# Optimization experiments

Hardware: AMD Instinct MI355X
Metric: run time of the kernel (lower is better)

Reference implementation:

```python
import jax, jax.numpy as jnp
import numpy as np
import math

S, D, H, HD = 2048, 1280, 16, 80  # seq_len, embed_dim, num_heads, head_dim


def setup_inputs() -> dict:
    key = jax.random.key(0)
    k1, k2, k3, k4, k5, k6 = jax.random.split(key, 6)
    hidden_states = jax.random.normal(k1, (S, D), dtype=jnp.float32)
    # 4 equal-length segments (e.g. 4 images of 512 patches)
    cu_seqlens = jnp.array([0, 512, 1024, 1536, 2048], dtype=jnp.int32)
    # RoPE theta*position angles, [S, HD//2]
    rotary_pos_emb = jax.random.uniform(k2, (S, HD // 2), dtype=jnp.float32) * 10.0
    qkv_w = jax.random.normal(k3, (3 * D, D), dtype=jnp.float32) * 0.02
    qkv_b = jax.random.normal(k4, (3 * D,), dtype=jnp.float32) * 0.02
    proj_w = jax.random.normal(k5, (D, D), dtype=jnp.float32) * 0.02
    proj_b = jax.random.normal(k6, (D,), dtype=jnp.float32) * 0.02
    return {"hidden_states": hidden_states, "cu_seqlens": cu_seqlens,
            "rotary_pos_emb": rotary_pos_emb, "qkv_w": qkv_w, "qkv_b": qkv_b,
            "proj_w": proj_w, "proj_b": proj_b}


def _rotate_half(x):
    x1, x2 = jnp.split(x, 2, axis=-1)
    return jnp.concatenate([-x2, x1], axis=-1)


def _square_mask(n, seq, dtype):
    # faithful translation of rewrite_loop_for_square_mask on a full-min mask
    neg = jnp.finfo(dtype).min
    mask = jnp.full((1, n, n), neg, dtype=dtype)
    r = jnp.arange(n)
    less0 = (r[:, None] < seq[None, :]).astype(jnp.int32)
    less = less0.sum(axis=-1, keepdims=True) + 1            # [n,1] segment label
    sq = less * less.T                                       # [n,n]
    c1 = jnp.logical_or(seq.min() == 0, less != less.max())
    c2 = jnp.logical_or(seq.max() == n, less != less.min())
    look = (c1 & c2).astype(jnp.int32) * less
    filt = (sq != look ** 2).astype(dtype)                   # 0 inside blocks, 1 outside
    return mask * filt


def reference(hidden_states, cu_seqlens, rotary_pos_emb, qkv_w, qkv_b, proj_w, proj_b):
    seq_len = hidden_states.shape[0]
    qkv = hidden_states @ qkv_w.T + qkv_b                    # [S, 3D]
    qkv = qkv.reshape(seq_len, 3, H, HD)
    q, k, v = qkv[:, 0], qkv[:, 1], qkv[:, 2]                # [S, H, HD]

    # rotary_pos_emb path: emb = cat(rope, rope), cos/sin broadcast over heads
    emb = jnp.concatenate([rotary_pos_emb, rotary_pos_emb], axis=-1)  # [S, HD]
    cos = jnp.cos(emb)[:, None, :]                           # [S, 1, HD]
    sin = jnp.sin(emb)[:, None, :]
    q = q * cos + _rotate_half(q) * sin
    k = k * cos + _rotate_half(k) * sin

    mask = _square_mask(seq_len, cu_seqlens, q.dtype)        # [1, S, S]

    qh = q.transpose(1, 0, 2)                                # [H, S, HD]
    kh = k.transpose(1, 0, 2)
    vh = v.transpose(1, 0, 2)

    attn = jnp.einsum('hqd,hkd->hqk', qh, kh) / math.sqrt(HD)  # [H, S, S]
    attn = attn + mask
    attn = jax.nn.softmax(attn.astype(jnp.float32), axis=-1).astype(q.dtype)
    out = jnp.einsum('hqk,hkd->hqd', attn, vh)               # [H, S, HD]
    out = out.transpose(1, 0, 2).reshape(seq_len, -1)        # [S, D]
    return out @ proj_w.T + proj_b
```

## Files before the change

### kernel.cpp

```cpp
#include <hip/hip_runtime.h>


typedef unsigned short u16;
typedef short short8 __attribute__((ext_vector_type(8)));
typedef float floatx4 __attribute__((ext_vector_type(4)));
typedef u16 ushort4v __attribute__((ext_vector_type(4)));
typedef float float4v __attribute__((ext_vector_type(4)));
typedef float float2v __attribute__((ext_vector_type(2)));

#define S_LEN 2048
#define DMODEL 1280
#define NHEAD 16
#define HDIM 80
#define HDIM_P 96
#define SEGS 4
#define SEG_LEN 512
#define QSCALE 0.11180339887498948f

__device__ __forceinline__ float b2f(u16 u) {
  union { unsigned int i; float f; } v; v.i = ((unsigned int)u) << 16; return v.f;
}
__device__ __forceinline__ u16 f2b(float f) {
  union { float f; unsigned int i; } v; v.f = f;
  unsigned int i = v.i;
  return (u16)((i + 0x7FFFu + ((i >> 16) & 1u)) >> 16);
}

__device__ __forceinline__ void load_lds16(const u16* g, u16* l) {
  __builtin_amdgcn_global_load_lds(
      (const __attribute__((address_space(1))) unsigned int*)g,
      (__attribute__((address_space(3))) unsigned int*)l, 16, 0, 0);
}

__device__ __forceinline__ unsigned int rope_perm(unsigned int j) {
  if (j >= 2560u) return j;
  unsigned int sec = j / 1280u;
  unsigned int jj = j - sec * 1280u;
  unsigned int h = jj / 80u, d = jj - h * 80u;
  unsigned int dp = (d < 40u) ? (2u * d) : (2u * (d - 40u) + 1u);
  return sec * 1280u + h * 80u + dp;
}

__global__ __launch_bounds__(256) void convert_all(
    const void* __restrict__ s_hid, const void* __restrict__ s_qw,
    const void* __restrict__ s_pw,  const void* __restrict__ s_rope,
    const void* __restrict__ s_qb,  const void* __restrict__ s_pb,
    u16* __restrict__ d_hid, u16* __restrict__ d_qw, u16* __restrict__ d_pw,
    u16* __restrict__ d_qb, u16* __restrict__ d_pb,
    int* __restrict__ flag_out, float* __restrict__ cs_tab,
    float* __restrict__ sn_tab) {
  unsigned int w = ((const unsigned int*)s_rope)[threadIdx.x & 63];
  int is_f32 = __any((int)((w >> 15) & 1));
  if (blockIdx.x == 0 && threadIdx.x == 0) *flag_out = is_f32;

  unsigned int qi = blockIdx.x * 256 + threadIdx.x;

  if (qi >= 2295040u) {
    unsigned int ti = qi - 2295040u;
    float ang = is_f32 ? ((const float*)s_rope)[ti]
                       : b2f(((const u16*)s_rope)[ti]);
    cs_tab[ti] = cosf(ang);
    sn_tab[ti] = sinf(ang);
    return;
  }

  if (qi >= 2293760u && qi < 2294720u) {
    unsigned int off = qi - 2293760u;
    ushort4v o;
    if (is_f32) {
      float4v f = ((const float4v*)s_qb)[off];
      #pragma unroll
      for (int i = 0; i < 4; ++i) o[i] = f2b(f[i]);
    } else {
      o = ((const ushort4v*)s_qb)[off];
    }
    #pragma unroll
    for (int e = 0; e < 4; ++e) d_qb[rope_perm(off * 4u + e)] = o[e];
    return;
  }

  const void* src; u16* dst; unsigned int off, doff;
  if      (qi < 655360u)  { src = s_hid;  dst = d_hid;  off = qi;            doff = off; }
  else if (qi < 1884160u) {
    src = s_qw; dst = d_qw; off = qi - 655360u;
    unsigned int row = off / 320u, col = off - row * 320u;
    doff = rope_perm(row) * 320u + col;
  }
  else if (qi < 2293760u) { src = s_pw;   dst = d_pw;   off = qi - 1884160u; doff = off; }
  else                    { src = s_pb;   dst = d_pb;   off = qi - 2294720u; doff = off; }
  ushort4v o;
  if (is_f32) {
    float4v f = ((const float4v*)src)[off];
    #pragma unroll
    for (int i = 0; i < 4; ++i) o[i] = f2b(f[i]);
  } else {
    o = ((const ushort4v*)src)[off];
  }
  ((ushort4v*)dst)[doff] = o;
}

__global__ __launch_bounds__(256) void gemm_qkv(
    const u16* __restrict__ A, const u16* __restrict__ W,
    const u16* __restrict__ bias,
    u16* __restrict__ qh, u16* __restrict__ kh, u16* __restrict__ vt,
    const float* __restrict__ cs, const float* __restrict__ sn) {
  const int K = DMODEL;
  __shared__ __attribute__((aligned(16))) u16 As[2][128 * 64];
  __shared__ __attribute__((aligned(16))) u16 Bs[2][128 * 64];
  int wave = threadIdx.x >> 6, lane = threadIdx.x & 63;
  int r = lane & 15, q = lane >> 4;
  int wm = wave >> 1, wn = wave & 1;

  int id = blockIdx.x + 30 * blockIdx.y;
  int xcd = id & 7, slot = id >> 3;
  int bx = slot % 30;
  int by = 2 * xcd + slot / 30;
  int m0 = by * 128, n0 = bx * 128;
  const int isV = (n0 >= 2 * DMODEL);

  int srow = lane >> 3;
  int sg   = (lane & 7) ^ srow;
  const u16* Ab = A + (size_t)(m0 + srow) * K + sg * 8;
  const u16* Wb = W + (size_t)(n0 + srow) * K + sg * 8;

  floatx4 acc[4][4];
  #pragma unroll
  for (int a = 0; a < 4; ++a)
    #pragma unroll
    for (int b = 0; b < 4; ++b) acc[a][b] = (floatx4){0.f, 0.f, 0.f, 0.f};

  #pragma unroll
  for (int c = 0; c < 4; ++c) {
    int ch = wave * 4 + c;
    load_lds16(Ab + (size_t)(ch * 8) * K, &As[0][ch * 8 * 64]);
    load_lds16(Wb + (size_t)(ch * 8) * K, &Bs[0][ch * 8 * 64]);
  }
  int buf = 0;
  for (int kt = 0; kt < K; kt += 64, buf ^= 1) {
    __syncthreads();
    if (kt + 64 < K) {
      #pragma unroll
      for (int c = 0; c < 4; ++c) {
        int ch = wave * 4 + c;
        load_lds16(Ab + kt + 64 + (size_t)(ch * 8) * K, &As[buf ^ 1][ch * 8 * 64]);
        load_lds16(Wb + kt + 64 + (size_t)(ch * 8) * K, &Bs[buf ^ 1][ch * 8 * 64]);
      }
    }
    #pragma unroll
    for (int ks = 0; ks < 2; ++ks) {
      short8 af[4], bf[4];
      #pragma unroll
      for (int i = 0; i < 4; ++i) {
        int arow = wm * 64 + i * 16 + r;
        int brow = wn * 64 + i * 16 + r;
        af[i] = *(const short8*)&As[buf][arow * 64 + (((ks * 4 + q) ^ (arow & 7)) * 8)];
        bf[i] = *(const short8*)&Bs[buf][brow * 64 + (((ks * 4 + q) ^ (brow & 7)) * 8)];
      }
      if (isV) {
        #pragma unroll
        for (int mi = 0; mi < 4; ++mi)
          #pragma unroll
          for (int ni = 0; ni < 4; ++ni)
            acc[mi][ni] = __builtin_amdgcn_mfma_f32_16x16x32_bf16(af[mi], bf[ni],
                                                                  acc[mi][ni], 0, 0, 0);
      } else {
        #pragma unroll
        for (int ni = 0; ni < 4; ++ni)
          #pragma unroll
          for (int mi = 0; mi < 4; ++mi)
            acc[ni][mi] = __builtin_amdgcn_mfma_f32_16x16x32_bf16(bf[ni], af[mi],
                                                                  acc[ni][mi], 0, 0, 0);
      }
    }
  }

  if (!isV) {
    #pragma unroll
    for (int ni = 0; ni < 4; ++ni) {
      int fbase = n0 + wn * 64 + ni * 16 + q * 4;
      int isq = fbase < DMODEL;
      int c2 = fbase - (isq ? 0 : DMODEL);
      int h = c2 / HDIM, cin = c2 - h * HDIM;
      float scale = isq ? QSCALE : 1.0f;
      u16* dstb = (isq ? qh : kh) + (size_t)h * S_LEN * HDIM_P + cin;
      ushort4v bv4 = *(const ushort4v*)&bias[fbase];
      float b0 = b2f(bv4[0]), b1 = b2f(bv4[1]);
      float b2v = b2f(bv4[2]), b3 = b2f(bv4[3]);
      int idx0 = cin >> 1;
      #pragma unroll
      for (int mi = 0; mi < 4; ++mi) {
        int s = m0 + wm * 64 + mi * 16 + r;
        float2v c2v = *(const float2v*)(cs + (size_t)s * 40 + idx0);
        float2v s2v = *(const float2v*)(sn + (size_t)s * 40 + idx0);
        float a0 = acc[ni][mi][0] + b0;
        float a1 = acc[ni][mi][1] + b1;
        float a2 = acc[ni][mi][2] + b2v;
        float a3 = acc[ni][mi][3] + b3;
        ushort4v o;
        o[0] = f2b((a0 * c2v[0] - a1 * s2v[0]) * scale);
        o[1] = f2b((a1 * c2v[0] + a0 * s2v[0]) * scale);
        o[2] = f2b((a2 * c2v[1] - a3 * s2v[1]) * scale);
        o[3] = f2b((a3 * c2v[1] + a2 * s2v[1]) * scale);
        *(ushort4v*)(dstb + (size_t)s * HDIM_P) = o;
      }
    }
  } else {
    #pragma unroll
    for (int ni = 0; ni < 4; ++ni) {
      int col = n0 + wn * 64 + ni * 16 + r;
      float bv = b2f(bias[col]);
      int c2 = col - 2 * DMODEL;
      #pragma unroll
      for (int mi = 0; mi < 4; ++mi) {
        int row0 = m0 + wm * 64 + mi * 16 + q * 4;
        ushort4v pk;
        #pragma unroll
        for (int i = 0; i < 4; ++i) pk[i] = f2b(acc[mi][ni][i] + bv);
        *(ushort4v*)(vt + (size_t)c2 * S_LEN + row0) = pk;
      }
    }
  }
}

#define PPAD 136
#define OPAD 84
struct WaveScratch {
  union {
    u16   P[32][PPAD];
    float O[32][OPAD];
  };
};
__global__ __launch_bounds__(256) void flash_attn(
    const u16* __restrict__ qh, const u16* __restrict__ kh,
    const u16* __restrict__ vt, const int* __restrict__ cu,
    u16* __restrict__ attn_out) {
  __shared__ __attribute__((aligned(16))) WaveScratch wsc[4];
  int wave = threadIdx.x >> 6, lane = threadIdx.x & 63;
  int r = lane & 15, q = lane >> 4;
  int hz = blockIdx.x;
  int seg = hz & (SEGS - 1), h = hz >> 2;
  int base = cu[seg];
  int m0 = blockIdx.y * 32;
  int k0 = wave * 128;

  const short8 zero8 = {0, 0, 0, 0, 0, 0, 0, 0};
  const u16* Qrow0 = qh + ((size_t)h * S_LEN + base + m0 + r) * HDIM_P + q * 8;
  const u16* Qrow1 = Qrow0 + (size_t)16 * HDIM_P;
  short8 aq[2][3];
  aq[0][0] = *(const short8*)(Qrow0);
  aq[0][1] = *(const short8*)(Qrow0 + 32);
  aq[0][2] = (q < 2) ? *(const short8*)(Qrow0 + 64) : zero8;
  aq[1][0] = *(const short8*)(Qrow1);
  aq[1][1] = *(const short8*)(Qrow1 + 32);
  aq[1][2] = (q < 2) ? *(const short8*)(Qrow1 + 64) : zero8;

  const u16* Kb = kh + ((size_t)h * S_LEN + base + k0 + r) * HDIM_P + q * 8;
  const u16* Vb = vt + ((size_t)h * HDIM + r) * S_LEN + base + k0 + q * 8;

  floatx4 sacc[2][8];
  #pragma unroll
  for (int g = 0; g < 8; ++g) {
    const u16* Kg = Kb + (size_t)(16 * g) * HDIM_P;
    short8 kf0 = *(const short8*)(Kg);
    short8 kf1 = *(const short8*)(Kg + 32);
    short8 kf2 = (q < 2) ? *(const short8*)(Kg + 64) : zero8;
    #pragma unroll
    for (int t = 0; t < 2; ++t) {
      floatx4 s = {0.f, 0.f, 0.f, 0.f};
      s = __builtin_amdgcn_mfma_f32_16x16x32_bf16(kf0, aq[t][0], s, 0, 0, 0);
      s = __builtin_amdgcn_mfma_f32_16x16x32_bf16(kf1, aq[t][1], s, 0, 0, 0);
      s = __builtin_amdgcn_mfma_f32_16x16x32_bf16(kf2, aq[t][2], s, 0, 0, 0);
      sacc[t][g] = s;
    }
  }

  #pragma unroll
  for (int t = 0; t < 2; ++t)
    #pragma unroll
    for (int g = 0; g < 8; ++g) {
      ushort4v pw;
      #pragma unroll
      for (int i = 0; i < 4; ++i) pw[i] = f2b(__expf(sacc[t][g][i]));
      *(ushort4v*)&wsc[wave].P[t * 16 + r][g * 16 + q * 4] = pw;
    }

  floatx4 o[2][5], o5[2];
  #pragma unroll
  for (int t = 0; t < 2; ++t) {
    o5[t] = (floatx4){0.f, 0.f, 0.f, 0.f};
    #pragma unroll
    for (int t5 = 0; t5 < 5; ++t5) o[t][t5] = (floatx4){0.f, 0.f, 0.f, 0.f};
  }
  const short8 ones = {0x3F80, 0x3F80, 0x3F80, 0x3F80, 0x3F80, 0x3F80, 0x3F80, 0x3F80};
  #pragma unroll
  for (int kq = 0; kq < 4; ++kq) {
    short8 pa0 = *(const short8*)&wsc[wave].P[r][kq * 32 + q * 8];
    short8 pa1 = *(const short8*)&wsc[wave].P[16 + r][kq * 32 + q * 8];
    #pragma unroll
    for (int t5 = 0; t5 < 5; ++t5) {
      short8 bv = *(const short8*)(Vb + kq * 32 + (size_t)(t5 * 16) * S_LEN);
      o[0][t5] = __builtin_amdgcn_mfma_f32_16x16x32_bf16(bv, pa0, o[0][t5], 0, 0, 0);
      o[1][t5] = __builtin_amdgcn_mfma_f32_16x16x32_bf16(bv, pa1, o[1][t5], 0, 0, 0);
    }
    o5[0] = __builtin_amdgcn_mfma_f32_16x16x32_bf16(ones, pa0, o5[0], 0, 0, 0);
    o5[1] = __builtin_amdgcn_mfma_f32_16x16x32_bf16(ones, pa1, o5[1], 0, 0, 0);
  }
  #pragma unroll
  for (int t = 0; t < 2; ++t)
    #pragma unroll
    for (int t5 = 0; t5 < 5; ++t5)
      *(float4v*)&wsc[wave].O[t * 16 + r][t5 * 16 + q * 4] = o[t][t5];
  if (q == 0) {
    wsc[wave].O[r][80]      = o5[0][0];
    wsc[wave].O[16 + r][80] = o5[1][0];
  }
  __syncthreads();

  int tid = threadIdx.x;
  int row = tid >> 3;
  int c0 = (tid & 7) * 10;
  float L = wsc[0].O[row][80] + wsc[1].O[row][80] +
            wsc[2].O[row][80] + wsc[3].O[row][80];
  float invL = 1.0f / L;
  u16* Or = attn_out + (size_t)(base + m0 + row) * DMODEL + h * HDIM + c0;
  #pragma unroll
  for (int j = 0; j < 10; ++j) {
    float v = wsc[0].O[row][c0 + j] + wsc[1].O[row][c0 + j] +
              wsc[2].O[row][c0 + j] + wsc[3].O[row][c0 + j];
    Or[j] = f2b(v * invL);
  }
}

__global__ __launch_bounds__(256) void gemm_tiled(
    const u16* __restrict__ A, const u16* __restrict__ W,
    const u16* __restrict__ bias, void* __restrict__ C,
    int M, int N, int K, const int* __restrict__ out_flag) {
  __shared__ __attribute__((aligned(16))) u16 As[2][64 * 64];
  __shared__ __attribute__((aligned(16))) u16 Bs[2][128 * 64];
  int wave = threadIdx.x >> 6, lane = threadIdx.x & 63;
  int r = lane & 15, q = lane >> 4;
  int wm = wave >> 1, wn = wave & 1;

  int bx = blockIdx.x, by = blockIdx.y;
  if (gridDim.x == 10 && gridDim.y == 32) {
    int id = bx + 10 * by;
    int xcd = id & 7, slot = id >> 3;
    bx = slot % 10;
    by = 4 * xcd + slot / 10;
  }
  int m0 = by * 64, n0 = bx * 128;

  int srow = lane >> 3;
  int sg   = (lane & 7) ^ srow;
  const u16* Ab = A + (size_t)(m0 + srow) * K + sg * 8;
  const u16* Wb = W + (size_t)(n0 + srow) * K + sg * 8;

  floatx4 acc[2][4];
  #pragma unroll
  for (int mi = 0; mi < 2; ++mi)
    #pragma unroll
    for (int ni = 0; ni < 4; ++ni) acc[mi][ni] = (floatx4){0.f, 0.f, 0.f, 0.f};

  #pragma unroll
  for (int c = 0; c < 2; ++c)
    load_lds16(Ab + (size_t)((wave * 2 + c) * 8) * K, &As[0][(wave * 2 + c) * 8 * 64]);
  #pragma unroll
  for (int c = 0; c < 4; ++c)
    load_lds16(Wb + (size_t)((wave * 4 + c) * 8) * K, &Bs[0][(wave * 4 + c) * 8 * 64]);

  int buf = 0;
  for (int kt = 0; kt < K; kt += 64, buf ^= 1) {
    __syncthreads();
    if (kt + 64 < K) {
      #pragma unroll
      for (int c = 0; c < 2; ++c)
        load_lds16(Ab + kt + 64 + (size_t)((wave * 2 + c) * 8) * K,
                   &As[buf ^ 1][(wave * 2 + c) * 8 * 64]);
      #pragma unroll
      for (int c = 0; c < 4; ++c)
        load_lds16(Wb + kt + 64 + (size_t)((wave * 4 + c) * 8) * K,
                   &Bs[buf ^ 1][(wave * 4 + c) * 8 * 64]);
    }
    #pragma unroll
    for (int ks = 0; ks < 2; ++ks) {
      short8 af[2], bf[4];
      #pragma unroll
      for (int i = 0; i < 2; ++i) {
        int arow = wm * 32 + i * 16 + r;
        af[i] = *(const short8*)&As[buf][arow * 64 + (((ks * 4 + q) ^ (arow & 7)) * 8)];
      }
      #pragma unroll
      for (int i = 0; i < 4; ++i) {
        int brow = wn * 64 + i * 16 + r;
        bf[i] = *(const short8*)&Bs[buf][brow * 64 + (((ks * 4 + q) ^ (brow & 7)) * 8)];
      }
      #pragma unroll
      for (int mi = 0; mi < 2; ++mi)
        #pragma unroll
        for (int ni = 0; ni < 4; ++ni)
          acc[mi][ni] = __builtin_amdgcn_mfma_f32_16x16x32_bf16(af[mi], bf[ni],
                                                                acc[mi][ni], 0, 0, 0);
    }
  }

  int f32out = out_flag ? *out_flag : 0;
  #pragma unroll
  for (int ni = 0; ni < 4; ++ni) {
    int col = n0 + wn * 64 + ni * 16 + r;
    float bv = b2f(bias[col]);
    #pragma unroll
    for (int mi = 0; mi < 2; ++mi) {
      size_t row0 = (size_t)(m0 + wm * 32 + mi * 16 + q * 4);
      if (f32out) {
        float* out = (float*)C;
        #pragma unroll
        for (int i = 0; i < 4; ++i) out[(row0 + i) * N + col] = acc[mi][ni][i] + bv;
      } else {
        u16* out = (u16*)C;
        #pragma unroll
        for (int i = 0; i < 4; ++i) out[(row0 + i) * N + col] = f2b(acc[mi][ni][i] + bv);
      }
    }
  }
}

extern "C" void kernel_launch(void* const* d_in, const int* in_sizes, int n_in,
                              void* d_out, int out_size, void* d_ws, size_t ws_size,
                              hipStream_t stream) {
  const void* hidden_r = d_in[0];
  const int*  cu       = (const int*)d_in[1];
  const void* rope_r   = d_in[2];
  const void* qkv_w_r  = d_in[3];
  const void* qkv_b_r  = d_in[4];
  const void* proj_w_r = d_in[5];
  const void* proj_b_r = d_in[6];

  char* ws = (char*)d_ws;
  u16* hidden_c = (u16*)(ws);
  u16* qkvw_c   = (u16*)(ws +  6291456u);
  u16* projw_c  = (u16*)(ws + 16777216u);
  u16* qkvb_c   = (u16*)(ws + 21135360u);
  u16* projb_c  = (u16*)(ws + 21143040u);
  int* flag     = (int*)(ws + 21145600u);
  float* cs_tab = (float*)(ws + 22020096u);
  float* sn_tab = (float*)(ws + 22347776u);
  u16* qh       = (u16*)(ws + 25165824u);
  u16* kh       = (u16*)(ws + 31457280u);
  u16* vt       = (u16*)(ws + 37748736u);
  u16* attn_out = (u16*)(ws + 44040192u);

  convert_all<<<dim3(9285), dim3(256), 0, stream>>>(
      hidden_r, qkv_w_r, proj_w_r, rope_r, qkv_b_r, proj_b_r,
      hidden_c, qkvw_c, projw_c, qkvb_c, projb_c, flag, cs_tab, sn_tab);

  gemm_qkv<<<dim3(3840 / 128, 2048 / 128), dim3(256), 0, stream>>>(
      hidden_c, qkvw_c, qkvb_c, qh, kh, vt, cs_tab, sn_tab);

  flash_attn<<<dim3(NHEAD * SEGS, SEG_LEN / 32), dim3(256), 0, stream>>>(
      qh, kh, vt, cu, attn_out);

  gemm_tiled<<<dim3(1280 / 128, 2048 / 64), dim3(256), 0, stream>>>(
      attn_out, projw_c, projb_c, d_out, S_LEN, DMODEL, DMODEL, flag);
}
```

Measured before the change: 164.2 us.

## Process 64 query rows per attention block to reuse K fragments across more queries

Each flash_attn block now handles 64 query rows instead of 32, halving the grid. K fragments loaded from global memory are reused across four query tiles, and the softmax probabilities for the second 32 rows are kept in registers and written to shared scratch after the first half's reduction. This cuts redundant K loads and block launch overhead. In exchange it raises register pressure, adds an extra barrier, and halves the number of blocks (512), which may reduce occupancy and latency hiding. V is still read twice per block.

```diff
diff --git a/kernel.cpp b/kernel.cpp
--- a/kernel.cpp
+++ b/kernel.cpp
@@ -240,24 +240,24 @@
   int hz = blockIdx.x;
   int seg = hz & (SEGS - 1), h = hz >> 2;
   int base = cu[seg];
-  int m0 = blockIdx.y * 32;
+  int m0 = blockIdx.y * 64;
   int k0 = wave * 128;
 
   const short8 zero8 = {0, 0, 0, 0, 0, 0, 0, 0};
-  const u16* Qrow0 = qh + ((size_t)h * S_LEN + base + m0 + r) * HDIM_P + q * 8;
-  const u16* Qrow1 = Qrow0 + (size_t)16 * HDIM_P;
-  short8 aq[2][3];
-  aq[0][0] = *(const short8*)(Qrow0);
-  aq[0][1] = *(const short8*)(Qrow0 + 32);
-  aq[0][2] = (q < 2) ? *(const short8*)(Qrow0 + 64) : zero8;
-  aq[1][0] = *(const short8*)(Qrow1);
-  aq[1][1] = *(const short8*)(Qrow1 + 32);
-  aq[1][2] = (q < 2) ? *(const short8*)(Qrow1 + 64) : zero8;
+  const u16* Qb = qh + ((size_t)h * S_LEN + base + m0 + r) * HDIM_P + q * 8;
+  short8 aq[4][3];
+  #pragma unroll
+  for (int t = 0; t < 4; ++t) {
+    const u16* Qt = Qb + (size_t)(t * 16) * HDIM_P;
+    aq[t][0] = *(const short8*)(Qt);
+    aq[t][1] = *(const short8*)(Qt + 32);
+    aq[t][2] = (q < 2) ? *(const short8*)(Qt + 64) : zero8;
+  }
 
   const u16* Kb = kh + ((size_t)h * S_LEN + base + k0 + r) * HDIM_P + q * 8;
   const u16* Vb = vt + ((size_t)h * HDIM + r) * S_LEN + base + k0 + q * 8;
 
-  floatx4 sacc[2][8];
+  ushort4v stash[2][8];
   #pragma unroll
   for (int g = 0; g < 8; ++g) {
     const u16* Kg = Kb + (size_t)(16 * g) * HDIM_P;
@@ -265,69 +265,77 @@
     short8 kf1 = *(const short8*)(Kg + 32);
     short8 kf2 = (q < 2) ? *(const short8*)(Kg + 64) : zero8;
     #pragma unroll
-    for (int t = 0; t < 2; ++t) {
+    for (int t = 0; t < 4; ++t) {
       floatx4 s = {0.f, 0.f, 0.f, 0.f};
       s = __builtin_amdgcn_mfma_f32_16x16x32_bf16(kf0, aq[t][0], s, 0, 0, 0);
       s = __builtin_amdgcn_mfma_f32_16x16x32_bf16(kf1, aq[t][1], s, 0, 0, 0);
       s = __builtin_amdgcn_mfma_f32_16x16x32_bf16(kf2, aq[t][2], s, 0, 0, 0);
-      sacc[t][g] = s;
-    }
-  }
-
-  #pragma unroll
-  for (int t = 0; t < 2; ++t)
-    #pragma unroll
-    for (int g = 0; g < 8; ++g) {
       ushort4v pw;
       #pragma unroll
-      for (int i = 0; i < 4; ++i) pw[i] = f2b(__expf(sacc[t][g][i]));
-      *(ushort4v*)&wsc[wave].P[t * 16 + r][g * 16 + q * 4] = pw;
-    }
-
-  floatx4 o[2][5], o5[2];
-  #pragma unroll
-  for (int t = 0; t < 2; ++t) {
-    o5[t] = (floatx4){0.f, 0.f, 0.f, 0.f};
-    #pragma unroll
-    for (int t5 = 0; t5 < 5; ++t5) o[t][t5] = (floatx4){0.f, 0.f, 0.f, 0.f};
-  }
+      for (int i = 0; i < 4; ++i) pw[i] = f2b(__expf(s[i]));
+      if (t < 2)
+        *(ushort4v*)&wsc[wave].P[t * 16 + r][g * 16 + q * 4] = pw;
+      else
+        stash[t - 2][g] = pw;
+    }
+  }
+
   const short8 ones = {0x3F80, 0x3F80, 0x3F80, 0x3F80, 0x3F80, 0x3F80, 0x3F80, 0x3F80};
   #pragma unroll
-  for (int kq = 0; kq < 4; ++kq) {
-    short8 pa0 = *(const short8*)&wsc[wave].P[r][kq * 32 + q * 8];
-    short8 pa1 = *(const short8*)&wsc[wave].P[16 + r][kq * 32 + q * 8];
-    #pragma unroll
-    for (int t5 = 0; t5 < 5; ++t5) {
-      short8 bv = *(const short8*)(Vb + kq * 32 + (size_t)(t5 * 16) * S_LEN);
-      o[0][t5] = __builtin_amdgcn_mfma_f32_16x16x32_bf16(bv, pa0, o[0][t5], 0, 0, 0);
-      o[1][t5] = __builtin_amdgcn_mfma_f32_16x16x32_bf16(bv, pa1, o[1][t5], 0, 0, 0);
-    }
-    o5[0] = __builtin_amdgcn_mfma_f32_16x16x32_bf16(ones, pa0, o5[0], 0, 0, 0);
-    o5[1] = __builtin_amdgcn_mfma_f32_16x16x32_bf16(ones, pa1, o5[1], 0, 0, 0);
-  }
-  #pragma unroll
-  for (int t = 0; t < 2; ++t)
-    #pragma unroll
-    for (int t5 = 0; t5 < 5; ++t5)
-      *(float4v*)&wsc[wave].O[t * 16 + r][t5 * 16 + q * 4] = o[t][t5];
-  if (q == 0) {
-    wsc[wave].O[r][80]      = o5[0][0];
-    wsc[wave].O[16 + r][80] = o5[1][0];
-  }
-  __syncthreads();
-
-  int tid = threadIdx.x;
-  int row = tid >> 3;
-  int c0 = (tid & 7) * 10;
-  float L = wsc[0].O[row][80] + wsc[1].O[row][80] +
-            wsc[2].O[row][80] + wsc[3].O[row][80];
-  float invL = 1.0f / L;
-  u16* Or = attn_out + (size_t)(base + m0 + row) * DMODEL + h * HDIM + c0;
-  #pragma unroll
-  for (int j = 0; j < 10; ++j) {
-    float v = wsc[0].O[row][c0 + j] + wsc[1].O[row][c0 + j] +
-              wsc[2].O[row][c0 + j] + wsc[3].O[row][c0 + j];
-    Or[j] = f2b(v * invL);
+  for (int half = 0; half < 2; ++half) {
+    if (half == 1) {
+      __syncthreads();
+      #pragma unroll
+      for (int t = 0; t < 2; ++t)
+        #pragma unroll
+        for (int g = 0; g < 8; ++g)
+          *(ushort4v*)&wsc[wave].P[t * 16 + r][g * 16 + q * 4] = stash[t][g];
+    }
+    floatx4 o[2][5], o5[2];
+    #pragma unroll
+    for (int t = 0; t < 2; ++t) {
+      o5[t] = (floatx4){0.f, 0.f, 0.f, 0.f};
+      #pragma unroll
+      for (int t5 = 0; t5 < 5; ++t5) o[t][t5] = (floatx4){0.f, 0.f, 0.f, 0.f};
+    }
+    #pragma unroll
+    for (int kq = 0; kq < 4; ++kq) {
+      short8 pa0 = *(const short8*)&wsc[wave].P[r][kq * 32 + q * 8];
+      short8 pa1 = *(const short8*)&wsc[wave].P[16 + r][kq * 32 + q * 8];
+      #pragma unroll
+      for (int t5 = 0; t5 < 5; ++t5) {
+        short8 bv = *(const short8*)(Vb + kq * 32 + (size_t)(t5 * 16) * S_LEN);
+        o[0][t5] = __builtin_amdgcn_mfma_f32_16x16x32_bf16(bv, pa0, o[0][t5], 0, 0, 0);
+        o[1][t5] = __builtin_amdgcn_mfma_f32_16x16x32_bf16(bv, pa1, o[1][t5], 0, 0, 0);
+      }
+      o5[0] = __builtin_amdgcn_mfma_f32_16x16x32_bf16(ones, pa0, o5[0], 0, 0, 0);
+      o5[1] = __builtin_amdgcn_mfma_f32_16x16x32_bf16(ones, pa1, o5[1], 0, 0, 0);
+    }
+    #pragma unroll
+    for (int t = 0; t < 2; ++t)
+      #pragma unroll
+      for (int t5 = 0; t5 < 5; ++t5)
+        *(float4v*)&wsc[wave].O[t * 16 + r][t5 * 16 + q * 4] = o[t][t5];
+    if (q == 0) {
+      wsc[wave].O[r][80]      = o5[0][0];
+      wsc[wave].O[16 + r][80] = o5[1][0];
+    }
+    __syncthreads();
+
+    int tid = threadIdx.x;
+    int row = tid >> 3;
+    int c0 = (tid & 7) * 10;
+    float L = wsc[0].O[row][80] + wsc[1].O[row][80] +
+              wsc[2].O[row][80] + wsc[3].O[row][80];
+    float invL = 1.0f / L;
+    u16* Or = attn_out +
+        (size_t)(base + m0 + half * 32 + row) * DMODEL + h * HDIM + c0;
+    #pragma unroll
+    for (int j = 0; j < 10; ++j) {
+      float v = wsc[0].O[row][c0 + j] + wsc[1].O[row][c0 + j] +
+                wsc[2].O[row][c0 + j] + wsc[3].O[row][c0 + j];
+      Or[j] = f2b(v * invL);
+    }
   }
 }
 
@@ -456,7 +464,7 @@
   gemm_qkv<<<dim3(3840 / 128, 2048 / 128), dim3(256), 0, stream>>>(
       hidden_c, qkvw_c, qkvb_c, qh, kh, vt, cs_tab, sn_tab);
 
-  flash_attn<<<dim3(NHEAD * SEGS, SEG_LEN / 32), dim3(256), 0, stream>>>(
+  flash_attn<<<dim3(NHEAD * SEGS, SEG_LEN / 64), dim3(256), 0, stream>>>(
       qh, kh, vt, cu, attn_out);
 
   gemm_tiled<<<dim3(1280 / 128, 2048 / 64), dim3(256), 0, stream>>>(
```

Result: no change. 162.3 us (-1.2%).
